# Kernel tuning notes

Measured on AMD Instinct MI355X. Metric: run time of the kernel, lower is better.

The kernel has to match this reference:

```python
import jax, jax.numpy as jnp
import numpy as np

SEM_ENC_DIM = 1024
SENT_HIDDEN_DIM = 1024
ATT_DIM = 512

def setup_inputs() -> dict:
    key = jax.random.key(0)
    ks = jax.random.split(key, 8)
    B, L = 64, 2048
    s = lambda d: 1.0 / np.sqrt(d)
    return {
        "sem_enc_output": jax.random.normal(ks[0], (B, L, SEM_ENC_DIM), dtype=jnp.float32),
        "dec_hidden_state": jax.random.normal(ks[1], (B, SENT_HIDDEN_DIM), dtype=jnp.float32),
        "W_enc": jax.random.uniform(ks[2], (SEM_ENC_DIM, ATT_DIM), jnp.float32, -s(SEM_ENC_DIM), s(SEM_ENC_DIM)),
        "b_enc": jax.random.uniform(ks[3], (ATT_DIM,), jnp.float32, -s(SEM_ENC_DIM), s(SEM_ENC_DIM)),
        "W_dec": jax.random.uniform(ks[4], (SENT_HIDDEN_DIM, ATT_DIM), jnp.float32, -s(SENT_HIDDEN_DIM), s(SENT_HIDDEN_DIM)),
        "b_dec": jax.random.uniform(ks[5], (ATT_DIM,), jnp.float32, -s(SENT_HIDDEN_DIM), s(SENT_HIDDEN_DIM)),
        "W_full": jax.random.uniform(ks[6], (ATT_DIM, 1), jnp.float32, -s(ATT_DIM), s(ATT_DIM)),
        "b_full": jax.random.uniform(ks[7], (1,), jnp.float32, -s(ATT_DIM), s(ATT_DIM)),
    }

def reference(sem_enc_output, dec_hidden_state, W_enc, b_enc, W_dec, b_dec, W_full, b_full):
    # enc projection: [B, L, att_dim]
    enc_proj = jnp.einsum('ble,ea->bla', sem_enc_output, W_enc) + b_enc
    # dec projection: [B, att_dim]
    dec_proj = dec_hidden_state @ W_dec + b_dec
    # broadcast add + tanh: [B, L, att_dim]
    joined = jnp.tanh(enc_proj + dec_proj[:, None, :])
    # scoring: [B, L]
    scores = (jnp.einsum('bla,a->bl', joined, W_full[:, 0]) + b_full[0])
    att_scores = jax.nn.softmax(scores, axis=1)
    # weighted sum over L of the PROJECTED encoder output (matches torch code)
    att_output = jnp.einsum('bl,bla->ba', att_scores, enc_proj)
    return (att_output, att_scores)
```

## Files before the change

### kernel.cpp

```cpp
#include <hip/hip_runtime.h>
#include <hip/hip_bf16.h>
#include <cstdint>
#include <cstddef>

#define BB   64
#define LL   2048
#define ED   1024
#define AD   512
#define BM   64
#define NCH  (LL / BM)
#define KST  32

typedef short  short4v __attribute__((ext_vector_type(4)));
typedef short  short8  __attribute__((ext_vector_type(8)));
typedef float  f32x4   __attribute__((ext_vector_type(4)));

__device__ __forceinline__ unsigned short f2bf(float x) {
  unsigned u = __float_as_uint(x);
  u += 0x7FFFu + ((u >> 16) & 1u);
  return (unsigned short)(u >> 16);
}

__device__ __forceinline__ short4v cvt4(f32x4 v) {
  union { short4v s; unsigned u[2]; } r;
  asm("v_cvt_pk_bf16_f32 %0, %1, %2" : "=v"(r.u[0]) : "v"(v[0]), "v"(v[1]));
  asm("v_cvt_pk_bf16_f32 %0, %1, %2" : "=v"(r.u[1]) : "v"(v[2]), "v"(v[3]));
  return r.s;
}

#define GLOAD_LDS16(gp, lp)                                                        \
  __builtin_amdgcn_global_load_lds(                                                \
      (const __attribute__((address_space(1))) unsigned int*)(gp),                 \
      (__attribute__((address_space(3))) unsigned int*)(lp), 16, 0, 0)

__global__ __launch_bounds__(512) void prep_kernel(
    const float* __restrict__ W_enc, const float* __restrict__ dec,
    const float* __restrict__ W_dec, const float* __restrict__ b_dec,
    unsigned short* __restrict__ Wb, float* __restrict__ dp) {
  const int blk = blockIdx.x, t = threadIdx.x;
  if (blk < BB) {
    const float* drow = dec + blk * ED;
    float a0 = 0.f, a1 = 0.f, a2 = 0.f, a3 = 0.f;
    for (int k = 0; k < ED; k += 4) {
      a0 = fmaf(drow[k],     W_dec[(k)     * AD + t], a0);
      a1 = fmaf(drow[k + 1], W_dec[(k + 1) * AD + t], a1);
      a2 = fmaf(drow[k + 2], W_dec[(k + 2) * AD + t], a2);
      a3 = fmaf(drow[k + 3], W_dec[(k + 3) * AD + t], a3);
    }
    dp[blk * AD + t] = (a0 + a1) + (a2 + a3) + b_dec[t];
  } else {
    const int base = (blk - BB) * 4096;
#pragma unroll
    for (int ii = 0; ii < 8; ii++) {
      const int o    = base + ii * 512 + t;
      const int ks   = o >> 14;
      const int cblk = (o >> 9) & 31;
      const int kg   = (o >> 7) & 3;
      const int r    = (o >> 3) & 15;
      const int j    = o & 7;
      const int k    = ks * 32 + kg * 8 + j;
      const int c    = cblk * 16 + r;
      Wb[o] = f2bf(W_enc[k * AD + c]);
    }
  }
}

__global__ __launch_bounds__(512, 4) void fused_kernel(
    const float* __restrict__ sem, const unsigned short* __restrict__ Wb,
    const float* __restrict__ dp, const float* __restrict__ b_enc,
    const float* __restrict__ Wf,
    float* __restrict__ raw_scores,
    float* __restrict__ ws_ms, float* __restrict__ ws_o) {

  __shared__ unsigned short Ab[2][2048];
  __shared__ unsigned short Bb[2][16384];

  const int t    = threadIdx.x;
  const int lane = t & 63;
  const int wn   = t >> 6;
  const int b    = blockIdx.y;
  const int chunk= blockIdx.x;
  const int l0   = chunk * BM;

  const int srow = t >> 3;
  const int skg  = t & 7;
  const float* aptr = sem + ((size_t)(b * LL + l0 + srow)) * ED + skg * 4;
  const int awr = (srow >> 4) * 512 + (skg >> 1) * 128 + (srow & 15) * 8 + (skg & 1) * 4;

  const unsigned short* bsrc = Wb + t * 8;

  const int arow = lane & 15;
  const int akg  = lane >> 4;
  const int afr  = lane * 8;
  const int bfr  = wn * 2048 + lane * 8;

  f32x4 acc[4][4];
#pragma unroll
  for (int i = 0; i < 4; i++)
#pragma unroll
    for (int j = 0; j < 4; j++) acc[i][j] = (f32x4)0.f;

#pragma unroll
  for (int i = 0; i < 4; i++)
    GLOAD_LDS16(bsrc + i * 4096, &Bb[0][i * 4096 + t * 8]);
  f32x4 pA = *(const f32x4*)(aptr);
  f32x4 qA = *(const f32x4*)(aptr + 32);
  *(short4v*)&Ab[0][awr] = cvt4(pA);
  asm volatile("s_waitcnt vmcnt(1) lgkmcnt(0)" ::: "memory");
  __builtin_amdgcn_sched_barrier(0);
  __builtin_amdgcn_s_barrier();

#define ITER(ks, CA, LA)                                                           \
  {                                                                                \
    const int cb = (ks) & 1, nb = ((ks) + 1) & 1;                                  \
    if ((ks) + 1 < KST) {                                                          \
      const unsigned short* bs = bsrc + ((ks) + 1) * 16384;                        \
      _Pragma("unroll")                                                            \
      for (int i = 0; i < 4; i++)                                                  \
        GLOAD_LDS16(bs + i * 4096, &Bb[nb][i * 4096 + t * 8]);                     \
    }                                                                              \
    __builtin_amdgcn_sched_barrier(0);          \
    if ((ks) + 1 < KST)                                                            \
      *(short4v*)&Ab[nb][awr] = cvt4(CA);          \
    if ((ks) + 2 < KST)                                                            \
      LA = *(const f32x4*)(aptr + ((ks) + 2) * 32);                                \
    short8 av[4], bv[4];                                                           \
    _Pragma("unroll")                                                              \
    for (int mf = 0; mf < 4; mf++)                                                 \
      av[mf] = *(const short8*)&Ab[cb][afr + mf * 512];                            \
    _Pragma("unroll")                                                              \
    for (int nf = 0; nf < 4; nf++)                                                 \
      bv[nf] = *(const short8*)&Bb[cb][bfr + nf * 512];                            \
    __builtin_amdgcn_s_setprio(1);                                                 \
    _Pragma("unroll")                                                              \
    for (int mf = 0; mf < 4; mf++)                                                 \
      _Pragma("unroll")                                                            \
      for (int nf = 0; nf < 4; nf++)                                               \
        acc[mf][nf] = __builtin_amdgcn_mfma_f32_16x16x32_bf16(av[mf], bv[nf], acc[mf][nf], 0, 0, 0); \
    __builtin_amdgcn_s_setprio(0);                                                 \
    if ((ks) + 2 < KST) {                                                          \
      asm volatile("s_waitcnt vmcnt(1) lgkmcnt(0)" ::: "memory");                  \
    } else {                                                                       \
      asm volatile("s_waitcnt vmcnt(0) lgkmcnt(0)" ::: "memory");                  \
    }                                                                              \
    __builtin_amdgcn_sched_barrier(0);                                             \
    __builtin_amdgcn_s_barrier();                                                  \
  }

  for (int kk = 0; kk < KST; kk += 2) {
    ITER(kk,     qA, pA);
    ITER(kk + 1, pA, qA);
  }
#undef ITER

  float* eb = (float*)&Bb[0][0];
  float (*sc_part)[8] = (float (*)[8])eb;
  float* weight       = eb + 512;

  float dpv[4], wfv[4], bev[4];
#pragma unroll
  for (int nf = 0; nf < 4; nf++) {
    const int c = wn * 64 + nf * 16 + arow;
    dpv[nf] = dp[b * AD + c];
    wfv[nf] = Wf[c];
    bev[nf] = b_enc[c];
  }
#pragma unroll
  for (int mf = 0; mf < 4; mf++) {
#pragma unroll
    for (int r = 0; r < 4; r++) {
      float p = 0.f;
#pragma unroll
      for (int nf = 0; nf < 4; nf++) {
        float e = acc[mf][nf][r] + bev[nf];
        acc[mf][nf][r] = e;
        float x = e + dpv[nf];
        float ex = __expf(2.f * x);
        float th = 1.f - 2.f / (ex + 1.f);
        p = fmaf(th, wfv[nf], p);
      }
      p += __shfl_xor(p, 1); p += __shfl_xor(p, 2);
      p += __shfl_xor(p, 4); p += __shfl_xor(p, 8);
      if (arow == 0) sc_part[mf * 16 + akg * 4 + r][wn] = p;
    }
  }
  __syncthreads();

  if (t < BM) {
    float s = sc_part[t][0] + sc_part[t][1] + sc_part[t][2] + sc_part[t][3]
            + sc_part[t][4] + sc_part[t][5] + sc_part[t][6] + sc_part[t][7];
    raw_scores[(size_t)b * LL + l0 + t] = s;
    float m = s;
#pragma unroll
    for (int off = 1; off < 64; off <<= 1) m = fmaxf(m, __shfl_xor(m, off));
    float w = __expf(s - m);
    weight[t] = w;
    float ss = w;
#pragma unroll
    for (int off = 1; off < 64; off <<= 1) ss += __shfl_xor(ss, off);
    if (t == 0) {
      ws_ms[(b * NCH + chunk) * 2]     = m;
      ws_ms[(b * NCH + chunk) * 2 + 1] = ss;
    }
  }
  __syncthreads();

  float wv[4][4];
#pragma unroll
  for (int mf = 0; mf < 4; mf++)
#pragma unroll
    for (int r = 0; r < 4; r++) wv[mf][r] = weight[mf * 16 + akg * 4 + r];
#pragma unroll
  for (int nf = 0; nf < 4; nf++) {
    float cp = 0.f;
#pragma unroll
    for (int mf = 0; mf < 4; mf++)
#pragma unroll
      for (int r = 0; r < 4; r++) cp = fmaf(wv[mf][r], acc[mf][nf][r], cp);
    cp += __shfl_xor(cp, 16);
    cp += __shfl_xor(cp, 32);
    if (lane < 16)
      ws_o[((size_t)b * NCH + chunk) * AD + wn * 64 + nf * 16 + lane] = cp;
  }
}

__global__ __launch_bounds__(256) void finalize_kernel(
    const float* __restrict__ ws_ms, const float* __restrict__ ws_o,
    float* __restrict__ out0, float* __restrict__ outS) {
  const int b = blockIdx.x, t = threadIdx.x;
  float ms[NCH], ss[NCH];
  float M = -1e30f;
#pragma unroll
  for (int i = 0; i < NCH; i++) {
    ms[i] = ws_ms[(b * NCH + i) * 2];
    ss[i] = ws_ms[(b * NCH + i) * 2 + 1];
    M = fmaxf(M, ms[i]);
  }
  float S = 0.f, w[NCH];
#pragma unroll
  for (int i = 0; i < NCH; i++) { w[i] = __expf(ms[i] - M); S = fmaf(ss[i], w[i], S); }
  const float invS = 1.f / S;
  for (int c = t; c < AD; c += 256) {
    float a = 0.f;
#pragma unroll
    for (int i = 0; i < NCH; i++) a = fmaf(ws_o[((size_t)b * NCH + i) * AD + c], w[i], a);
    out0[b * AD + c] = a * invS;
  }
  for (int l = t; l < LL; l += 256) {
    float r = outS[(size_t)b * LL + l];
    outS[(size_t)b * LL + l] = __expf(r - M) * invS;
  }
}

extern "C" void kernel_launch(void* const* d_in, const int* in_sizes, int n_in,
                              void* d_out, int out_size, void* d_ws, size_t ws_size,
                              hipStream_t stream) {
  const float* sem    = (const float*)d_in[0];
  const float* dec    = (const float*)d_in[1];
  const float* W_enc  = (const float*)d_in[2];
  const float* b_enc  = (const float*)d_in[3];
  const float* W_dec  = (const float*)d_in[4];
  const float* b_dec  = (const float*)d_in[5];
  const float* W_full = (const float*)d_in[6];

  float* out0 = (float*)d_out;
  float* outS = out0 + BB * AD;

  char* ws = (char*)d_ws;
  unsigned short* Wb = (unsigned short*)ws;
  float* dpw   = (float*)(ws + (1 << 20));
  float* ws_ms = (float*)(ws + (1 << 20) + (128 << 10));
  float* ws_o  = (float*)(ws + (1 << 20) + (144 << 10));

  prep_kernel<<<BB + 128, 512, 0, stream>>>(W_enc, dec, W_dec, b_dec, Wb, dpw);
  dim3 g1(NCH, BB);
  fused_kernel<<<g1, 512, 0, stream>>>(sem, Wb, dpw, b_enc, W_full, outS, ws_ms, ws_o);
  finalize_kernel<<<BB, 256, 0, stream>>>(ws_ms, ws_o, out0, outS);
}
```

Measured before the change: 278.9 us.

## Load W_enc fragments directly from global into registers, drop B LDS staging

The pre-swizzled bf16 W_enc tiles are now read straight from global memory (L2-resident) into MFMA operand registers instead of being staged through double-buffered shared memory. The A tile stage is widened to 64 K per iteration with two MFMA sub-steps, which halves the number of barriers. This removes about 64KB of LDS per block, which may raise occupancy, and cuts barrier and LDS traffic. The cost is exposed global-load latency on B right before the MFMAs, with no prefetch, and more per-wave L2 traffic, since each wave now fetches B itself rather than sharing one copy per block. The epilogue scratch area is moved into the A buffer, which is now 16KB, so it must fit.

Measured after the change: 300.2 us. 1.08x slower.

```diff
diff --git a/kernel.cpp b/kernel.cpp
--- a/kernel.cpp
+++ b/kernel.cpp
@@ -9,9 +9,8 @@
 #define AD   512
 #define BM   64
 #define NCH  (LL / BM)
-#define KST  32
-
-typedef short  short4v __attribute__((ext_vector_type(4)));
+#define KS2  16
+
 typedef short  short8  __attribute__((ext_vector_type(8)));
 typedef float  f32x4   __attribute__((ext_vector_type(4)));
 
@@ -21,17 +20,14 @@
   return (unsigned short)(u >> 16);
 }
 
-__device__ __forceinline__ short4v cvt4(f32x4 v) {
-  union { short4v s; unsigned u[2]; } r;
-  asm("v_cvt_pk_bf16_f32 %0, %1, %2" : "=v"(r.u[0]) : "v"(v[0]), "v"(v[1]));
-  asm("v_cvt_pk_bf16_f32 %0, %1, %2" : "=v"(r.u[1]) : "v"(v[2]), "v"(v[3]));
+__device__ __forceinline__ short8 cvt8(f32x4 lo, f32x4 hi) {
+  union { short8 s; unsigned u[4]; } r;
+  asm("v_cvt_pk_bf16_f32 %0, %1, %2" : "=v"(r.u[0]) : "v"(lo[0]), "v"(lo[1]));
+  asm("v_cvt_pk_bf16_f32 %0, %1, %2" : "=v"(r.u[1]) : "v"(lo[2]), "v"(lo[3]));
+  asm("v_cvt_pk_bf16_f32 %0, %1, %2" : "=v"(r.u[2]) : "v"(hi[0]), "v"(hi[1]));
+  asm("v_cvt_pk_bf16_f32 %0, %1, %2" : "=v"(r.u[3]) : "v"(hi[2]), "v"(hi[3]));
   return r.s;
 }
-
-#define GLOAD_LDS16(gp, lp)                                                        \
-  __builtin_amdgcn_global_load_lds(                                                \
-      (const __attribute__((address_space(1))) unsigned int*)(gp),                 \
-      (__attribute__((address_space(3))) unsigned int*)(lp), 16, 0, 0)
 
 __global__ __launch_bounds__(512) void prep_kernel(
     const float* __restrict__ W_enc, const float* __restrict__ dec,
@@ -72,8 +68,7 @@
     float* __restrict__ raw_scores,
     float* __restrict__ ws_ms, float* __restrict__ ws_o) {
 
-  __shared__ unsigned short Ab[2][2048];
-  __shared__ unsigned short Bb[2][16384];
+  __shared__ unsigned short Ab[2][4096];
 
   const int t    = threadIdx.x;
   const int lane = t & 63;
@@ -84,15 +79,13 @@
 
   const int srow = t >> 3;
   const int skg  = t & 7;
-  const float* aptr = sem + ((size_t)(b * LL + l0 + srow)) * ED + skg * 4;
-  const int awr = (srow >> 4) * 512 + (skg >> 1) * 128 + (srow & 15) * 8 + (skg & 1) * 4;
-
-  const unsigned short* bsrc = Wb + t * 8;
+  const float* aptr = sem + ((size_t)(b * LL + l0 + srow)) * ED + skg * 8;
+  const int awr = (skg >> 2) * 2048 + (srow >> 4) * 512 + (skg & 3) * 128 + (srow & 15) * 8;
 
   const int arow = lane & 15;
   const int akg  = lane >> 4;
   const int afr  = lane * 8;
-  const int bfr  = wn * 2048 + lane * 8;
+  const unsigned short* wbb = Wb + wn * 2048 + lane * 8;
 
   f32x4 acc[4][4];
 #pragma unroll
@@ -100,46 +93,82 @@
 #pragma unroll
     for (int j = 0; j < 4; j++) acc[i][j] = (f32x4)0.f;
 
-#pragma unroll
-  for (int i = 0; i < 4; i++)
-    GLOAD_LDS16(bsrc + i * 4096, &Bb[0][i * 4096 + t * 8]);
-  f32x4 pA = *(const f32x4*)(aptr);
-  f32x4 qA = *(const f32x4*)(aptr + 32);
-  *(short4v*)&Ab[0][awr] = cvt4(pA);
-  asm volatile("s_waitcnt vmcnt(1) lgkmcnt(0)" ::: "memory");
+  f32x4 tA0 = *(const f32x4*)(aptr);
+  f32x4 tA1 = *(const f32x4*)(aptr + 4);
+  f32x4 qA0 = *(const f32x4*)(aptr + 64);
+  f32x4 qA1 = *(const f32x4*)(aptr + 68);
+  f32x4 pA0, pA1;
+  *(short8*)&Ab[0][awr] = cvt8(tA0, tA1);
+  asm volatile("s_waitcnt lgkmcnt(0)" ::: "memory");
   __builtin_amdgcn_sched_barrier(0);
   __builtin_amdgcn_s_barrier();
 
-#define ITER(ks, CA, LA)                                                           \
+#define ITER(ks, CA0, CA1, LA0, LA1)                                               \
   {                                                                                \
     const int cb = (ks) & 1, nb = ((ks) + 1) & 1;                                  \
-    if ((ks) + 1 < KST) {                                                          \
-      const unsigned short* bs = bsrc + ((ks) + 1) * 16384;                        \
-      _Pragma("unroll")                                                            \
-      for (int i = 0; i < 4; i++)                                                  \
-        GLOAD_LDS16(bs + i * 4096, &Bb[nb][i * 4096 + t * 8]);                     \
+    const unsigned short* wq = wbb + (size_t)(2 * (ks)) * 16384;                   \
+    short8 bv0, bv1, bv2, bv3;                                                     \
+    bv0 = *(const short8*)(wq);                                                    \
+    bv1 = *(const short8*)(wq + 512);                                              \
+    bv2 = *(const short8*)(wq + 1024);                                             \
+    bv3 = *(const short8*)(wq + 1536);                                             \
+    if ((ks) + 2 < KS2) {                                                          \
+      const float* ap = aptr + ((ks) + 2) * 64;                                    \
+      LA0 = *(const f32x4*)(ap);                                                   \
+      LA1 = *(const f32x4*)(ap + 4);                                               \
     }                                                                              \
-    __builtin_amdgcn_sched_barrier(0);          \
-    if ((ks) + 1 < KST)                                                            \
-      *(short4v*)&Ab[nb][awr] = cvt4(CA);          \
-    if ((ks) + 2 < KST)                                                            \
-      LA = *(const f32x4*)(aptr + ((ks) + 2) * 32);                                \
-    short8 av[4], bv[4];                                                           \
-    _Pragma("unroll")                                                              \
-    for (int mf = 0; mf < 4; mf++)                                                 \
-      av[mf] = *(const short8*)&Ab[cb][afr + mf * 512];                            \
-    _Pragma("unroll")                                                              \
-    for (int nf = 0; nf < 4; nf++)                                                 \
-      bv[nf] = *(const short8*)&Bb[cb][bfr + nf * 512];                            \
+    if ((ks) + 1 < KS2)                                                            \
+      *(short8*)&Ab[nb][awr] = cvt8(CA0, CA1);         \
+    short8 av0 = *(const short8*)&Ab[cb][afr];                                     \
+    short8 av1 = *(const short8*)&Ab[cb][afr + 512];                               \
+    short8 av2 = *(const short8*)&Ab[cb][afr + 1024];                              \
+    short8 av3 = *(const short8*)&Ab[cb][afr + 1536];                              \
     __builtin_amdgcn_s_setprio(1);                                                 \
-    _Pragma("unroll")                                                              \
-    for (int mf = 0; mf < 4; mf++)                                                 \
-      _Pragma("unroll")                                                            \
-      for (int nf = 0; nf < 4; nf++)                                               \
-        acc[mf][nf] = __builtin_amdgcn_mfma_f32_16x16x32_bf16(av[mf], bv[nf], acc[mf][nf], 0, 0, 0); \
+    acc[0][0] = __builtin_amdgcn_mfma_f32_16x16x32_bf16(av0, bv0, acc[0][0],0,0,0);\
+    acc[1][0] = __builtin_amdgcn_mfma_f32_16x16x32_bf16(av1, bv0, acc[1][0],0,0,0);\
+    acc[2][0] = __builtin_amdgcn_mfma_f32_16x16x32_bf16(av2, bv0, acc[2][0],0,0,0);\
+    acc[3][0] = __builtin_amdgcn_mfma_f32_16x16x32_bf16(av3, bv0, acc[3][0],0,0,0);\
+    acc[0][1] = __builtin_amdgcn_mfma_f32_16x16x32_bf16(av0, bv1, acc[0][1],0,0,0);\
+    acc[1][1] = __builtin_amdgcn_mfma_f32_16x16x32_bf16(av1, bv1, acc[1][1],0,0,0);\
+    acc[2][1] = __builtin_amdgcn_mfma_f32_16x16x32_bf16(av2, bv1, acc[2][1],0,0,0);\
+    acc[3][1] = __builtin_amdgcn_mfma_f32_16x16x32_bf16(av3, bv1, acc[3][1],0,0,0);\
+    acc[0][2] = __builtin_amdgcn_mfma_f32_16x16x32_bf16(av0, bv2, acc[0][2],0,0,0);\
+    acc[1][2] = __builtin_amdgcn_mfma_f32_16x16x32_bf16(av1, bv2, acc[1][2],0,0,0);\
+    acc[2][2] = __builtin_amdgcn_mfma_f32_16x16x32_bf16(av2, bv2, acc[2][2],0,0,0);\
+    acc[3][2] = __builtin_amdgcn_mfma_f32_16x16x32_bf16(av3, bv2, acc[3][2],0,0,0);\
+    acc[0][3] = __builtin_amdgcn_mfma_f32_16x16x32_bf16(av0, bv3, acc[0][3],0,0,0);\
+    acc[1][3] = __builtin_amdgcn_mfma_f32_16x16x32_bf16(av1, bv3, acc[1][3],0,0,0);\
+    acc[2][3] = __builtin_amdgcn_mfma_f32_16x16x32_bf16(av2, bv3, acc[2][3],0,0,0);\
+    acc[3][3] = __builtin_amdgcn_mfma_f32_16x16x32_bf16(av3, bv3, acc[3][3],0,0,0);\
     __builtin_amdgcn_s_setprio(0);                                                 \
-    if ((ks) + 2 < KST) {                                                          \
-      asm volatile("s_waitcnt vmcnt(1) lgkmcnt(0)" ::: "memory");                  \
+    bv0 = *(const short8*)(wq + 16384);                                            \
+    bv1 = *(const short8*)(wq + 16384 + 512);                                      \
+    bv2 = *(const short8*)(wq + 16384 + 1024);                                     \
+    bv3 = *(const short8*)(wq + 16384 + 1536);                                     \
+    av0 = *(const short8*)&Ab[cb][afr + 2048];                                     \
+    av1 = *(const short8*)&Ab[cb][afr + 2560];                                     \
+    av2 = *(const short8*)&Ab[cb][afr + 3072];                                     \
+    av3 = *(const short8*)&Ab[cb][afr + 3584];                                     \
+    __builtin_amdgcn_s_setprio(1);                                                 \
+    acc[0][0] = __builtin_amdgcn_mfma_f32_16x16x32_bf16(av0, bv0, acc[0][0],0,0,0);\
+    acc[1][0] = __builtin_amdgcn_mfma_f32_16x16x32_bf16(av1, bv0, acc[1][0],0,0,0);\
+    acc[2][0] = __builtin_amdgcn_mfma_f32_16x16x32_bf16(av2, bv0, acc[2][0],0,0,0);\
+    acc[3][0] = __builtin_amdgcn_mfma_f32_16x16x32_bf16(av3, bv0, acc[3][0],0,0,0);\
+    acc[0][1] = __builtin_amdgcn_mfma_f32_16x16x32_bf16(av0, bv1, acc[0][1],0,0,0);\
+    acc[1][1] = __builtin_amdgcn_mfma_f32_16x16x32_bf16(av1, bv1, acc[1][1],0,0,0);\
+    acc[2][1] = __builtin_amdgcn_mfma_f32_16x16x32_bf16(av2, bv1, acc[2][1],0,0,0);\
+    acc[3][1] = __builtin_amdgcn_mfma_f32_16x16x32_bf16(av3, bv1, acc[3][1],0,0,0);\
+    acc[0][2] = __builtin_amdgcn_mfma_f32_16x16x32_bf16(av0, bv2, acc[0][2],0,0,0);\
+    acc[1][2] = __builtin_amdgcn_mfma_f32_16x16x32_bf16(av1, bv2, acc[1][2],0,0,0);\
+    acc[2][2] = __builtin_amdgcn_mfma_f32_16x16x32_bf16(av2, bv2, acc[2][2],0,0,0);\
+    acc[3][2] = __builtin_amdgcn_mfma_f32_16x16x32_bf16(av3, bv2, acc[3][2],0,0,0);\
+    acc[0][3] = __builtin_amdgcn_mfma_f32_16x16x32_bf16(av0, bv3, acc[0][3],0,0,0);\
+    acc[1][3] = __builtin_amdgcn_mfma_f32_16x16x32_bf16(av1, bv3, acc[1][3],0,0,0);\
+    acc[2][3] = __builtin_amdgcn_mfma_f32_16x16x32_bf16(av2, bv3, acc[2][3],0,0,0);\
+    acc[3][3] = __builtin_amdgcn_mfma_f32_16x16x32_bf16(av3, bv3, acc[3][3],0,0,0);\
+    __builtin_amdgcn_s_setprio(0);                                                 \
+    if ((ks) + 2 < KS2) {                                                          \
+      asm volatile("s_waitcnt vmcnt(2) lgkmcnt(0)" ::: "memory");                  \
     } else {                                                                       \
       asm volatile("s_waitcnt vmcnt(0) lgkmcnt(0)" ::: "memory");                  \
     }                                                                              \
@@ -147,13 +176,13 @@
     __builtin_amdgcn_s_barrier();                                                  \
   }
 
-  for (int kk = 0; kk < KST; kk += 2) {
-    ITER(kk,     qA, pA);
-    ITER(kk + 1, pA, qA);
+  for (int kk = 0; kk < KS2; kk += 2) {
+    ITER(kk,     qA0, qA1, pA0, pA1);
+    ITER(kk + 1, pA0, pA1, qA0, qA1);
   }
 #undef ITER
 
-  float* eb = (float*)&Bb[0][0];
+  float* eb = (float*)&Ab[0][0];
   float (*sc_part)[8] = (float (*)[8])eb;
   float* weight       = eb + 512;
 
```

## Double L-tile to 128 rows with 1024-thread blocks and triple-buffered W_enc

Applied to the files above, without the earlier changes.

Doubles the per-block row tile to 128 rows and launches 16 waves split 2x8 over M and N, so each bf16 W_enc slice loaded into LDS feeds twice as many rows. The W_enc tile is triple-buffered, with prefetch two k-steps ahead, and the A tile stays double-buffered. The epilogue gains extra LDS reductions to combine scores and partial outputs across the two M-waves. This halves the chunks per batch and the global W_enc traffic, but cuts the grid in half, raises LDS use and limits occupancy.

After: 294.5 us. 1.06x slower.

```diff
diff --git a/kernel.cpp b/kernel.cpp
--- a/kernel.cpp
+++ b/kernel.cpp
@@ -7,7 +7,7 @@
 #define LL   2048
 #define ED   1024
 #define AD   512
-#define BM   64
+#define BM   128
 #define NCH  (LL / BM)
 #define KST  32
 
@@ -65,19 +65,21 @@
   }
 }
 
-__global__ __launch_bounds__(512, 4) void fused_kernel(
+__global__ __launch_bounds__(1024, 4) void fused_kernel(
     const float* __restrict__ sem, const unsigned short* __restrict__ Wb,
     const float* __restrict__ dp, const float* __restrict__ b_enc,
     const float* __restrict__ Wf,
     float* __restrict__ raw_scores,
     float* __restrict__ ws_ms, float* __restrict__ ws_o) {
 
-  __shared__ unsigned short Ab[2][2048];
-  __shared__ unsigned short Bb[2][16384];
+  __shared__ unsigned short Ab[2][4096];
+  __shared__ unsigned short Bb[3][16384];
 
   const int t    = threadIdx.x;
   const int lane = t & 63;
-  const int wn   = t >> 6;
+  const int wave = t >> 6;
+  const int wm   = wave >> 3;
+  const int wnn  = wave & 7;
   const int b    = blockIdx.y;
   const int chunk= blockIdx.x;
   const int l0   = chunk * BM;
@@ -91,8 +93,8 @@
 
   const int arow = lane & 15;
   const int akg  = lane >> 4;
-  const int afr  = lane * 8;
-  const int bfr  = wn * 2048 + lane * 8;
+  const int afr  = wm * 2048 + lane * 8;
+  const int bfr  = wnn * 2048 + lane * 8;
 
   f32x4 acc[4][4];
 #pragma unroll
@@ -100,37 +102,37 @@
 #pragma unroll
     for (int j = 0; j < 4; j++) acc[i][j] = (f32x4)0.f;
 
-#pragma unroll
-  for (int i = 0; i < 4; i++)
-    GLOAD_LDS16(bsrc + i * 4096, &Bb[0][i * 4096 + t * 8]);
+  GLOAD_LDS16(bsrc,                 &Bb[0][t * 8]);
+  GLOAD_LDS16(bsrc + 8192,          &Bb[0][8192 + t * 8]);
+  GLOAD_LDS16(bsrc + 16384,         &Bb[1][t * 8]);
+  GLOAD_LDS16(bsrc + 16384 + 8192,  &Bb[1][8192 + t * 8]);
+  __builtin_amdgcn_sched_barrier(0);
   f32x4 pA = *(const f32x4*)(aptr);
   f32x4 qA = *(const f32x4*)(aptr + 32);
   *(short4v*)&Ab[0][awr] = cvt4(pA);
-  asm volatile("s_waitcnt vmcnt(1) lgkmcnt(0)" ::: "memory");
+  asm volatile("s_waitcnt lgkmcnt(0)" ::: "memory");
   __builtin_amdgcn_sched_barrier(0);
   __builtin_amdgcn_s_barrier();
 
-#define ITER(ks, CA, LA)                                                           \
+#define ITER(ks, BR, BW, AR, AW, CA, LA)                                           \
   {                                                                                \
-    const int cb = (ks) & 1, nb = ((ks) + 1) & 1;                                  \
-    if ((ks) + 1 < KST) {                                                          \
-      const unsigned short* bs = bsrc + ((ks) + 1) * 16384;                        \
-      _Pragma("unroll")                                                            \
-      for (int i = 0; i < 4; i++)                                                  \
-        GLOAD_LDS16(bs + i * 4096, &Bb[nb][i * 4096 + t * 8]);                     \
+    if ((ks) + 2 < KST) {                                                          \
+      const unsigned short* bs = bsrc + (size_t)((ks) + 2) * 16384;                \
+      GLOAD_LDS16(bs,        &Bb[BW][t * 8]);                                      \
+      GLOAD_LDS16(bs + 8192, &Bb[BW][8192 + t * 8]);                               \
     }                                                                              \
     __builtin_amdgcn_sched_barrier(0);          \
     if ((ks) + 1 < KST)                                                            \
-      *(short4v*)&Ab[nb][awr] = cvt4(CA);          \
+      *(short4v*)&Ab[AW][awr] = cvt4(CA);                                          \
     if ((ks) + 2 < KST)                                                            \
       LA = *(const f32x4*)(aptr + ((ks) + 2) * 32);                                \
     short8 av[4], bv[4];                                                           \
     _Pragma("unroll")                                                              \
     for (int mf = 0; mf < 4; mf++)                                                 \
-      av[mf] = *(const short8*)&Ab[cb][afr + mf * 512];                            \
+      av[mf] = *(const short8*)&Ab[AR][afr + mf * 512];                            \
     _Pragma("unroll")                                                              \
     for (int nf = 0; nf < 4; nf++)                                                 \
-      bv[nf] = *(const short8*)&Bb[cb][bfr + nf * 512];                            \
+      bv[nf] = *(const short8*)&Bb[BR][bfr + nf * 512];                            \
     __builtin_amdgcn_s_setprio(1);                                                 \
     _Pragma("unroll")                                                              \
     for (int mf = 0; mf < 4; mf++)                                                 \
@@ -138,29 +140,34 @@
       for (int nf = 0; nf < 4; nf++)                                               \
         acc[mf][nf] = __builtin_amdgcn_mfma_f32_16x16x32_bf16(av[mf], bv[nf], acc[mf][nf], 0, 0, 0); \
     __builtin_amdgcn_s_setprio(0);                                                 \
-    if ((ks) + 2 < KST) {                                                          \
-      asm volatile("s_waitcnt vmcnt(1) lgkmcnt(0)" ::: "memory");                  \
-    } else {                                                                       \
-      asm volatile("s_waitcnt vmcnt(0) lgkmcnt(0)" ::: "memory");                  \
-    }                                                                              \
+    asm volatile("s_waitcnt lgkmcnt(0)" ::: "memory");                             \
     __builtin_amdgcn_sched_barrier(0);                                             \
     __builtin_amdgcn_s_barrier();                                                  \
   }
 
-  for (int kk = 0; kk < KST; kk += 2) {
-    ITER(kk,     qA, pA);
-    ITER(kk + 1, pA, qA);
-  }
+  for (int kk = 0; kk < 30; kk += 6) {
+    ITER(kk + 0, 0, 2, 0, 1, qA, pA)
+    ITER(kk + 1, 1, 0, 1, 0, pA, qA)
+    ITER(kk + 2, 2, 1, 0, 1, qA, pA)
+    ITER(kk + 3, 0, 2, 1, 0, pA, qA)
+    ITER(kk + 4, 1, 0, 0, 1, qA, pA)
+    ITER(kk + 5, 2, 1, 1, 0, pA, qA)
+  }
+  ITER(30, 0, 2, 0, 1, qA, pA)
+  ITER(31, 1, 0, 1, 0, pA, qA)
 #undef ITER
 
   float* eb = (float*)&Bb[0][0];
-  float (*sc_part)[8] = (float (*)[8])eb;
-  float* weight       = eb + 512;
+  float (*sc_part)[8]  = (float (*)[8])eb;
+  float* scores_lds    = eb + 1024;
+  float* weight        = eb + 1152;
+  float (*o_lds)[AD]   = (float (*)[AD])(eb + 1280);
+  float* bcv           = eb + 2304;
 
   float dpv[4], wfv[4], bev[4];
 #pragma unroll
   for (int nf = 0; nf < 4; nf++) {
-    const int c = wn * 64 + nf * 16 + arow;
+    const int c = wnn * 64 + nf * 16 + arow;
     dpv[nf] = dp[b * AD + c];
     wfv[nf] = Wf[c];
     bev[nf] = b_enc[c];
@@ -181,7 +188,7 @@
       }
       p += __shfl_xor(p, 1); p += __shfl_xor(p, 2);
       p += __shfl_xor(p, 4); p += __shfl_xor(p, 8);
-      if (arow == 0) sc_part[mf * 16 + akg * 4 + r][wn] = p;
+      if (arow == 0) sc_part[wm * 64 + mf * 16 + akg * 4 + r][wnn] = p;
     }
   }
   __syncthreads();
@@ -189,27 +196,32 @@
   if (t < BM) {
     float s = sc_part[t][0] + sc_part[t][1] + sc_part[t][2] + sc_part[t][3]
             + sc_part[t][4] + sc_part[t][5] + sc_part[t][6] + sc_part[t][7];
+    scores_lds[t] = s;
     raw_scores[(size_t)b * LL + l0 + t] = s;
-    float m = s;
+  }
+  __syncthreads();
+  if (t < 64) {
+    float m = fmaxf(scores_lds[t], scores_lds[t + 64]);
 #pragma unroll
     for (int off = 1; off < 64; off <<= 1) m = fmaxf(m, __shfl_xor(m, off));
-    float w = __expf(s - m);
-    weight[t] = w;
-    float ss = w;
-#pragma unroll
-    for (int off = 1; off < 64; off <<= 1) ss += __shfl_xor(ss, off);
-    if (t == 0) {
-      ws_ms[(b * NCH + chunk) * 2]     = m;
-      ws_ms[(b * NCH + chunk) * 2 + 1] = ss;
-    }
-  }
-  __syncthreads();
+    if (t == 0) bcv[0] = m;
+  }
+  __syncthreads();
+  const float m_c = bcv[0];
+  if (t < BM) weight[t] = __expf(scores_lds[t] - m_c);
+  __syncthreads();
+  if (t < 64) {
+    float s = weight[t] + weight[t + 64];
+#pragma unroll
+    for (int off = 1; off < 64; off <<= 1) s += __shfl_xor(s, off);
+    if (t == 0) bcv[1] = s;
+  }
 
   float wv[4][4];
 #pragma unroll
   for (int mf = 0; mf < 4; mf++)
 #pragma unroll
-    for (int r = 0; r < 4; r++) wv[mf][r] = weight[mf * 16 + akg * 4 + r];
+    for (int r = 0; r < 4; r++) wv[mf][r] = weight[wm * 64 + mf * 16 + akg * 4 + r];
 #pragma unroll
   for (int nf = 0; nf < 4; nf++) {
     float cp = 0.f;
@@ -219,8 +231,14 @@
       for (int r = 0; r < 4; r++) cp = fmaf(wv[mf][r], acc[mf][nf][r], cp);
     cp += __shfl_xor(cp, 16);
     cp += __shfl_xor(cp, 32);
-    if (lane < 16)
-      ws_o[((size_t)b * NCH + chunk) * AD + wn * 64 + nf * 16 + lane] = cp;
+    if (lane < 16) o_lds[wm][wnn * 64 + nf * 16 + lane] = cp;
+  }
+  __syncthreads();
+  if (t < AD)
+    ws_o[((size_t)b * NCH + chunk) * AD + t] = o_lds[0][t] + o_lds[1][t];
+  if (t == 0) {
+    ws_ms[(b * NCH + chunk) * 2]     = m_c;
+    ws_ms[(b * NCH + chunk) * 2 + 1] = bcv[1];
   }
 }
 
@@ -270,10 +288,10 @@
   unsigned short* Wb = (unsigned short*)ws;
   float* dpw   = (float*)(ws + (1 << 20));
   float* ws_ms = (float*)(ws + (1 << 20) + (128 << 10));
-  float* ws_o  = (float*)(ws + (1 << 20) + (144 << 10));
+  float* ws_o  = (float*)(ws + (1 << 20) + (136 << 10));
 
   prep_kernel<<<BB + 128, 512, 0, stream>>>(W_enc, dec, W_dec, b_dec, Wb, dpw);
   dim3 g1(NCH, BB);
-  fused_kernel<<<g1, 512, 0, stream>>>(sem, Wb, dpw, b_enc, W_full, outS, ws_ms, ws_o);
+  fused_kernel<<<g1, 1024, 0, stream>>>(sem, Wb, dpw, b_enc, W_full, outS, ws_ms, ws_o);
   finalize_kernel<<<BB, 256, 0, stream>>>(ws_ms, ws_o, out0, outS);
 }
```
